# Optimization experiments

Hardware: AMD Instinct MI355X
Metric: run time of the kernel (lower is better)

## Reference

```python
import jax, jax.numpy as jnp
import numpy as np

E = 1024  # embed_dim
H = 16    # num_heads
D = E // H  # head_dim


def setup_inputs() -> dict:
    key = jax.random.key(0)
    ks = jax.random.split(key, 9)
    s = 0.02
    return {
        "hidden_state": jax.random.normal(ks[0], (4, 1024, E), jnp.float32),
        "Wq": jax.random.normal(ks[1], (H, D, E), jnp.float32) * s,
        "bq": jax.random.normal(ks[2], (H, D), jnp.float32) * s,
        "Wk": jax.random.normal(ks[3], (H, D, E), jnp.float32) * s,
        "bk": jax.random.normal(ks[4], (H, D), jnp.float32) * s,
        "Wv": jax.random.normal(ks[5], (H, D, E), jnp.float32) * s,
        "bv": jax.random.normal(ks[6], (H, D), jnp.float32) * s,
        "Wo": jax.random.normal(ks[7], (E, E), jnp.float32) * s,
        "bo": jax.random.normal(ks[8], (E,), jnp.float32) * s,
    }


def _mha(x, Wq, bq, Wk, bk, Wv, bv, Wo, bo):
    # Per-head linear projections (torch Linear: y = x W^T + b), batched over heads.
    q = jnp.einsum("bse,hde->bhsd", x, Wq) + bq[None, :, None, :]
    k = jnp.einsum("bse,hde->bhsd", x, Wk) + bk[None, :, None, :]
    v = jnp.einsum("bse,hde->bhsd", x, Wv) + bv[None, :, None, :]
    scores = jnp.einsum("bhsd,bhtd->bhst", q, k) / jnp.sqrt(jnp.asarray(D, x.dtype))
    w = jax.nn.softmax(scores, axis=-1)  # F.softmax default -> last dim
    o = jnp.einsum("bhst,bhtd->bhsd", w, v)
    # concat heads along last dim: [B,S,H*D] in head order (matches torch.cat)
    B, _, S, _ = o.shape
    o = jnp.transpose(o, (0, 2, 1, 3)).reshape(B, S, H * D)
    return o @ Wo.T + bo


def reference(hidden_state, Wq, bq, Wk, bk, Wv, bv, Wo, bo):
    return _mha(hidden_state, Wq, bq, Wk, bk, Wv, bv, Wo, bo)
```

## Files before the change

### kernel.cpp

```cpp
#include <hip/hip_runtime.h>
#include <hip/hip_bf16.h>
#include <stdint.h>

#define E_DIM 1024
#define H_NUM 16
#define D_DIM 64
#define B_NUM 4
#define S_LEN 1024

typedef __attribute__((ext_vector_type(8))) short bf16x8;
typedef __attribute__((ext_vector_type(4))) short bf16x4;
typedef __attribute__((ext_vector_type(4))) float f32x4;

#define SOFTMAX_C2 0.18033688011112042f

__device__ inline ushort f2b(float x) {
    __hip_bfloat16 h = __float2bfloat16(x);
    return *(ushort*)&h;
}
__device__ inline float b2f(ushort u) {
    __hip_bfloat16 h = *(__hip_bfloat16*)&u;
    return __bfloat162float(h);
}
__device__ inline uint pk2(float a, float b) {
    __hip_bfloat162 h = __float22bfloat162_rn(make_float2(a, b));
    return *(uint*)&h;
}

__device__ inline void gld16(const ushort* g, ushort* l) {
    __builtin_amdgcn_global_load_lds((const __attribute__((address_space(1))) void*)g,
                                     (__attribute__((address_space(3))) void*)l, 16, 0, 0);
}

__global__ __launch_bounds__(256)
void convert_all(const float* __restrict__ X,  const float* __restrict__ Wq,
                 const float* __restrict__ Wk, const float* __restrict__ Wv,
                 const float* __restrict__ Wo,
                 ushort* __restrict__ Xb, ushort* __restrict__ Wcat,
                 ushort* __restrict__ Wob)
{
    const int bid = blockIdx.x;
    const float* src; ushort* dst; size_t off;
    if (bid < 4096)      { src = X;  dst = Xb;   off = (size_t)bid * 1024; }
    else if (bid < 5120) { src = Wq; dst = Wcat;              off = (size_t)(bid - 4096) * 1024; }
    else if (bid < 6144) { src = Wk; dst = Wcat + (1u << 20); off = (size_t)(bid - 5120) * 1024; }
    else if (bid < 7168) { src = Wv; dst = Wcat + (2u << 20); off = (size_t)(bid - 6144) * 1024; }
    else                 { src = Wo; dst = Wob;               off = (size_t)(bid - 7168) * 1024; }
    const size_t i = off + (size_t)threadIdx.x * 4;
    float4 v = *(const float4*)&src[i];
    ushort4 o;
    o.x = f2b(v.x); o.y = f2b(v.y); o.z = f2b(v.z); o.w = f2b(v.w);
    *(ushort4*)&dst[i] = o;
}

__global__ __launch_bounds__(256, 3)
void gemm_qkv(const ushort* __restrict__ A, const ushort* __restrict__ Bw,
              const float* __restrict__ b0, const float* __restrict__ b1,
              const float* __restrict__ b2,
              ushort* __restrict__ Qb, ushort* __restrict__ Kb,
              ushort* __restrict__ Vt_g, int K)
{
    __shared__ __align__(16) ushort SM[24576];
    ushort* As = SM;
    ushort* Bs = SM + 16384;

    const int tid  = threadIdx.x;
    const int wave = tid >> 6;
    const int lane = tid & 63;
    const int quad = lane >> 4;
    const int l16  = lane & 15;
    const int wm   = wave & 1;
    const int wn   = wave >> 1;
    const int m0   = blockIdx.x * 128;
    const int n0   = blockIdx.y * 64;

    f32x4 acc[4][2] = {};

    auto stageA = [&](int buf, int k0) {
#pragma unroll
        for (int i = 0; i < 4; ++i) {
            const int e   = i * 256 + tid;
            const int row = e >> 3;
            const int gc8 = ((e & 7) ^ (row & 7)) * 8;
            gld16(&A[(size_t)(m0 + row) * K + k0 + gc8], &As[buf * 8192 + e * 8]);
        }
    };
    auto stageB = [&](int buf, int k0) {
#pragma unroll
        for (int i = 0; i < 2; ++i) {
            const int e   = i * 256 + tid;
            const int row = e >> 3;
            const int gc8 = ((e & 7) ^ (row & 7)) * 8;
            gld16(&Bw[(size_t)(n0 + row) * K + k0 + gc8], &Bs[buf * 4096 + e * 8]);
        }
    };

    stageA(0, 0); stageB(0, 0);
    __syncthreads();

    const int nk = K >> 6;
    const int xa = (l16 & 7) * 8;
    for (int ki = 0; ki < nk; ++ki) {
        const int cur = ki & 1;
        if (ki + 1 < nk) { stageA(cur ^ 1, (ki + 1) << 6); stageB(cur ^ 1, (ki + 1) << 6); }

#pragma unroll
        for (int ks = 0; ks < 2; ++ks) {
            const int lc = (ks * 32 + quad * 8) ^ xa;
            bf16x8 af[4], bf[2];
#pragma unroll
            for (int mi = 0; mi < 4; ++mi)
                af[mi] = *(const bf16x8*)&As[cur * 8192 + (wm * 64 + mi * 16 + l16) * 64 + lc];
#pragma unroll
            for (int ni = 0; ni < 2; ++ni)
                bf[ni] = *(const bf16x8*)&Bs[cur * 4096 + (wn * 32 + ni * 16 + l16) * 64 + lc];
#pragma unroll
            for (int mi = 0; mi < 4; ++mi)
#pragma unroll
                for (int ni = 0; ni < 2; ++ni)
                    acc[mi][ni] = __builtin_amdgcn_mfma_f32_16x16x32_bf16(af[mi], bf[ni], acc[mi][ni], 0, 0, 0);
        }
        __syncthreads();
    }

    const int seg   = n0 >> 10;
    const int cbase = n0 & 1023;
    const float* bp = (seg == 0) ? b0 : (seg == 1) ? b1 : b2;
    const float scl = (seg == 0) ? SOFTMAX_C2 : 1.0f;

    if (seg < 2) {
        ushort* T = SM;
#pragma unroll
        for (int ni = 0; ni < 2; ++ni) {
            const int nloc = wn * 32 + ni * 16 + l16;
            const float bv = bp[cbase + nloc];
#pragma unroll
            for (int mi = 0; mi < 4; ++mi)
#pragma unroll
                for (int r = 0; r < 4; ++r)
                    T[(wm * 64 + mi * 16 + quad * 4 + r) * 72 + nloc] =
                        f2b((acc[mi][ni][r] + bv) * scl);
        }
        __syncthreads();
        ushort* dst = (seg == 0) ? Qb : Kb;
        const int row = tid >> 1, half = tid & 1;
        const ushort* s = &T[row * 72 + half * 32];
        ushort* d = &dst[(size_t)(m0 + row) * 1024 + cbase + half * 32];
#pragma unroll
        for (int j = 0; j < 4; ++j)
            *(uint4*)(d + j * 8) = *(const uint4*)(s + j * 8);
    } else {
        ushort* Tt = SM;
        const int hh = cbase >> 6;
        const int b  = m0 >> 10, sbase = m0 & 1023;
#pragma unroll
        for (int ni = 0; ni < 2; ++ni) {
            const int nloc = wn * 32 + ni * 16 + l16;
            const float bv = bp[cbase + nloc];
#pragma unroll
            for (int mi = 0; mi < 4; ++mi) {
                const int mloc = wm * 64 + mi * 16 + quad * 4;
                ushort4 pk;
                pk.x = f2b(acc[mi][ni][0] + bv);
                pk.y = f2b(acc[mi][ni][1] + bv);
                pk.z = f2b(acc[mi][ni][2] + bv);
                pk.w = f2b(acc[mi][ni][3] + bv);
                *(ushort4*)&Tt[nloc * 136 + mloc] = pk;
            }
        }
        __syncthreads();
        const int nrow = tid >> 2, qtr = tid & 3;
        const ushort* s = &Tt[nrow * 136 + qtr * 32];
        ushort* d = &Vt_g[(((size_t)(b * 16 + hh)) * 64 + nrow) * 1024 + sbase + qtr * 32];
#pragma unroll
        for (int j = 0; j < 4; ++j)
            *(uint4*)(d + j * 8) = *(const uint4*)(s + j * 8);
    }
}

__global__ __launch_bounds__(256, 8)
void attention6(const ushort* __restrict__ Qg, const ushort* __restrict__ Kg,
                const ushort* __restrict__ Vg,
                ushort* __restrict__ Opart, float* __restrict__ Lpart)
{
    __shared__ ushort Kb[2][32][72];
    __shared__ ushort Vb[2][64][40];

    const int tid  = threadIdx.x;
    const int w    = tid >> 6;
    const int lane = tid & 63;
    const int quad = lane >> 4;
    const int l16  = lane & 15;

    const int qt = blockIdx.x;
    const int bh = blockIdx.y;
    const int th = blockIdx.z;
    const int b  = bh >> 4;
    const int h  = bh & 15;
    const size_t tbase = ((size_t)b * S_LEN) * E_DIM + (size_t)h * D_DIM;
    const size_t vbase = (size_t)bh * D_DIM * S_LEN;
    const int t0 = th * 512;

    const ushort* qrow = Qg + tbase + (size_t)(qt * 64 + w * 16 + l16) * E_DIM + quad * 8;
    bf16x8 qf[2];
    qf[0] = *(const bf16x8*)qrow;
    qf[1] = *(const bf16x8*)(qrow + 32);

    {
        const int kr = tid >> 3, kc = (tid & 7) * 8;
        *(uint4*)&Kb[0][kr][kc] = *(const uint4*)&Kg[tbase + (size_t)(t0 + kr) * E_DIM + kc];
        const int vr = tid >> 2, vc = (tid & 3) * 8;
        *(uint4*)&Vb[0][vr][vc] = *(const uint4*)&Vg[vbase + (size_t)vr * S_LEN + t0 + vc];
    }
    __syncthreads();

    float lq = 0.0f;
    f32x4 oacc[4] = {};

    for (int kt = 0; kt < 16; ++kt) {
        const int cur = kt & 1;

        uint4 kpre, vpre;
        const int kr = tid >> 3, kc = (tid & 7) * 8;
        const int vr = tid >> 2, vc = (tid & 3) * 8;
        if (kt < 15) {
            const int tg = t0 + (kt + 1) * 32;
            kpre = *(const uint4*)&Kg[tbase + (size_t)(tg + kr) * E_DIM + kc];
            vpre = *(const uint4*)&Vg[vbase + (size_t)vr * S_LEN + tg + vc];
        }

        f32x4 sacc[2] = {};
#pragma unroll
        for (int mt = 0; mt < 2; ++mt)
#pragma unroll
            for (int ks = 0; ks < 2; ++ks) {
                bf16x8 kf = *(const bf16x8*)&Kb[cur][mt * 16 + l16][ks * 32 + quad * 8];
                sacc[mt] = __builtin_amdgcn_mfma_f32_16x16x32_bf16(kf, qf[ks], sacc[mt], 0, 0, 0);
            }

        bf16x4 pf[2];
        float rs = 0.0f;
#pragma unroll
        for (int mt = 0; mt < 2; ++mt) {
            float p0 = exp2f(sacc[mt][0]);
            float p1 = exp2f(sacc[mt][1]);
            float p2 = exp2f(sacc[mt][2]);
            float p3 = exp2f(sacc[mt][3]);
            rs += (p0 + p1) + (p2 + p3);
            union { uint uu[2]; bf16x4 v; } pk;
            pk.uu[0] = pk2(p0, p1);
            pk.uu[1] = pk2(p2, p3);
            pf[mt] = pk.v;
        }
        lq += rs;

#pragma unroll
        for (int nb = 0; nb < 4; ++nb)
#pragma unroll
            for (int kb = 0; kb < 2; ++kb) {
                bf16x4 vf = *(const bf16x4*)&Vb[cur][nb * 16 + l16][kb * 16 + quad * 4];
                oacc[nb] = __builtin_amdgcn_mfma_f32_16x16x16bf16_1k(pf[kb], vf, oacc[nb], 0, 0, 0);
            }

        if (kt < 15) {
            const int nxt = cur ^ 1;
            *(uint4*)&Kb[nxt][kr][kc] = kpre;
            *(uint4*)&Vb[nxt][vr][vc] = vpre;
        }
        __syncthreads();
    }

    lq += __shfl_xor(lq, 16);
    lq += __shfl_xor(lq, 32);
    const size_t obase = ((size_t)(th * 64 + bh)) * S_LEN;
    if (lane < 16)
        Lpart[obase + qt * 64 + w * 16 + l16] = lq;

    ushort* T = &Kb[0][0][0];
#pragma unroll
    for (int nb = 0; nb < 4; ++nb)
#pragma unroll
        for (int r = 0; r < 4; ++r)
            T[(w * 16 + quad * 4 + r) * 72 + nb * 16 + l16] = f2b(oacc[nb][r]);
    __syncthreads();
    {
        const int row = tid >> 2, c16 = (tid & 3) * 16;
        const ushort* s = &T[row * 72 + c16];
        ushort* d = &Opart[(obase + qt * 64 + row) * 64 + c16];
        *(uint4*)(d)     = *(const uint4*)(s);
        *(uint4*)(d + 8) = *(const uint4*)(s + 8);
    }
}

__global__ __launch_bounds__(256, 3)
void gemm_out(const ushort* __restrict__ Opart, const float* __restrict__ Lpart,
              const ushort* __restrict__ Bw, const float* __restrict__ bias,
              float* __restrict__ Cout)
{
    __shared__ __align__(16) ushort SM[26624];
    ushort* As = SM;
    ushort* Bs = SM + 18432;

    const int tid  = threadIdx.x;
    const int wave = tid >> 6;
    const int lane = tid & 63;
    const int quad = lane >> 4;
    const int l16  = lane & 15;
    const int wm   = wave & 1;
    const int wn   = wave >> 1;
    const int m0   = blockIdx.x * 128;
    const int n0   = blockIdx.y * 64;

    const int arow = tid >> 1;
    const int ah   = (tid & 1) * 32;
    const int m    = m0 + arow;
    const int ab   = m >> 10;
    const int as   = m & 1023;

    f32x4 acc[4][2] = {};

    auto loadA = [&](int ki, uint4* o0, uint4* o1, float* linv) {
        const int bh = ab * 16 + ki;
        const size_t p0 = ((size_t)bh * 1024 + as) * 64 + ah;
        const size_t p1 = ((size_t)(64 + bh) * 1024 + as) * 64 + ah;
#pragma unroll
        for (int j = 0; j < 4; ++j) {
            o0[j] = *(const uint4*)&Opart[p0 + j * 8];
            o1[j] = *(const uint4*)&Opart[p1 + j * 8];
        }
        const float l0 = Lpart[(size_t)bh * 1024 + as];
        const float l1 = Lpart[(size_t)(64 + bh) * 1024 + as];
        *linv = 1.0f / (l0 + l1);
    };
    auto writeA = [&](int buf, const uint4* o0, const uint4* o1, float linv) {
        ushort* dst = &As[buf * 9216 + arow * 72 + ah];
#pragma unroll
        for (int j = 0; j < 4; ++j) {
            const ushort* a = (const ushort*)&o0[j];
            const ushort* c = (const ushort*)&o1[j];
            union { uint uu[4]; uint4 v; } pk;
            pk.uu[0] = pk2((b2f(a[0]) + b2f(c[0])) * linv, (b2f(a[1]) + b2f(c[1])) * linv);
            pk.uu[1] = pk2((b2f(a[2]) + b2f(c[2])) * linv, (b2f(a[3]) + b2f(c[3])) * linv);
            pk.uu[2] = pk2((b2f(a[4]) + b2f(c[4])) * linv, (b2f(a[5]) + b2f(c[5])) * linv);
            pk.uu[3] = pk2((b2f(a[6]) + b2f(c[6])) * linv, (b2f(a[7]) + b2f(c[7])) * linv);
            *(uint4*)(dst + j * 8) = pk.v;
        }
    };
    auto stageB = [&](int buf, int k0) {
#pragma unroll
        for (int i = 0; i < 2; ++i) {
            const int e   = i * 256 + tid;
            const int row = e >> 3;
            const int gc8 = ((e & 7) ^ (row & 7)) * 8;
            gld16(&Bw[(size_t)(n0 + row) * 1024 + k0 + gc8], &Bs[buf * 4096 + e * 8]);
        }
    };

    {
        uint4 o0[4], o1[4]; float linv;
        loadA(0, o0, o1, &linv);
        writeA(0, o0, o1, linv);
        stageB(0, 0);
    }
    __syncthreads();

    const int xa = (l16 & 7) * 8;
    for (int ki = 0; ki < 16; ++ki) {
        const int cur = ki & 1;

        uint4 o0[4], o1[4]; float linv;
        if (ki + 1 < 16) {
            loadA(ki + 1, o0, o1, &linv);
            stageB(cur ^ 1, (ki + 1) << 6);
        }

#pragma unroll
        for (int ks = 0; ks < 2; ++ks) {
            const int lcB = (ks * 32 + quad * 8) ^ xa;
            bf16x8 af[4], bf[2];
#pragma unroll
            for (int mi = 0; mi < 4; ++mi)
                af[mi] = *(const bf16x8*)&As[cur * 9216 + (wm * 64 + mi * 16 + l16) * 72 + ks * 32 + quad * 8];
#pragma unroll
            for (int ni = 0; ni < 2; ++ni)
                bf[ni] = *(const bf16x8*)&Bs[cur * 4096 + (wn * 32 + ni * 16 + l16) * 64 + lcB];
#pragma unroll
            for (int mi = 0; mi < 4; ++mi)
#pragma unroll
                for (int ni = 0; ni < 2; ++ni)
                    acc[mi][ni] = __builtin_amdgcn_mfma_f32_16x16x32_bf16(af[mi], bf[ni], acc[mi][ni], 0, 0, 0);
        }

        if (ki + 1 < 16) writeA(cur ^ 1, o0, o1, linv);
        __syncthreads();
    }

    float* Tf = (float*)SM;
    float bv[2];
#pragma unroll
    for (int ni = 0; ni < 2; ++ni)
        bv[ni] = bias[n0 + wn * 32 + ni * 16 + l16];
#pragma unroll
    for (int p = 0; p < 2; ++p) {
        if (wm == p) {
#pragma unroll
            for (int ni = 0; ni < 2; ++ni) {
                const int nloc = wn * 32 + ni * 16 + l16;
#pragma unroll
                for (int mi = 0; mi < 4; ++mi)
#pragma unroll
                    for (int r = 0; r < 4; ++r)
                        Tf[(mi * 16 + quad * 4 + r) * 68 + nloc] = acc[mi][ni][r] + bv[ni];
            }
        }
        __syncthreads();
        const int row = tid >> 2, c16 = (tid & 3) * 16;
        const float* s = &Tf[row * 68 + c16];
        float* d = &Cout[(size_t)(m0 + p * 64 + row) * 1024 + n0 + c16];
#pragma unroll
        for (int j = 0; j < 4; ++j)
            *(float4*)(d + j * 4) = *(const float4*)(s + j * 4);
        __syncthreads();
    }
}

extern "C" void kernel_launch(void* const* d_in, const int* in_sizes, int n_in,
                              void* d_out, int out_size, void* d_ws, size_t ws_size,
                              hipStream_t stream)
{
    (void)in_sizes; (void)n_in; (void)out_size; (void)ws_size;

    const float* X  = (const float*)d_in[0];
    const float* Wq = (const float*)d_in[1];
    const float* bq = (const float*)d_in[2];
    const float* Wk = (const float*)d_in[3];
    const float* bk = (const float*)d_in[4];
    const float* Wv = (const float*)d_in[5];
    const float* bv = (const float*)d_in[6];
    const float* Wo = (const float*)d_in[7];
    const float* bo = (const float*)d_in[8];

    const size_t MEG = 1u << 20;
    ushort* ws    = (ushort*)d_ws;
    ushort* Xb    = ws;
    ushort* Wcat  = ws + 4 * MEG;
    ushort* Wob   = ws + 7 * MEG;
    ushort* Qb    = ws + 8 * MEG;
    ushort* Kb    = ws + 12 * MEG;
    ushort* Vtg   = ws + 16 * MEG;
    ushort* Opart = ws + 20 * MEG;
    float*  Lpart = (float*)(ws + 28 * MEG);

    dim3 blk(256);

    convert_all<<<8192, blk, 0, stream>>>(X, Wq, Wk, Wv, Wo, Xb, Wcat, Wob);

    gemm_qkv<<<dim3(32, 48), blk, 0, stream>>>(Xb, Wcat, bq, bk, bv,
                                               Qb, Kb, Vtg, E_DIM);

    attention6<<<dim3(16, 64, 2), blk, 0, stream>>>(Qb, Kb, Vtg, Opart, Lpart);

    gemm_out<<<dim3(32, 16), blk, 0, stream>>>(Opart, Lpart, Wob, bo,
                                               (float*)d_out);
}
```

Measured before the change: 201.5 us.

## Stage K tiles via direct global-to-LDS loads with swizzle; remap grid; shrink output GEMM tile

The attention kernel now stages K tiles with a direct global-to-LDS load helper (gld16) into an XOR-swizzled LDS layout, so K no longer passes through registers. It also flattens the grid to 1D with a remapped block index that groups the query tiles of one (batch, head, half) together for cache locality. The output GEMM drops from 128x64 to 64x64 tiles with one 16-row slice per wave, doubling the block count and raising the occupancy hint. Smaller tiles reduce per-block reuse of the weight tile, and correctness depends on gld16 ordering against the barrier.

```diff
diff --git a/kernel.cpp b/kernel.cpp
--- a/kernel.cpp
+++ b/kernel.cpp
@@ -179,12 +179,11 @@
 }
 
 __global__ __launch_bounds__(256, 8)
-void attention6(const ushort* __restrict__ Qg, const ushort* __restrict__ Kg,
+void attention7(const ushort* __restrict__ Qg, const ushort* __restrict__ Kg,
                 const ushort* __restrict__ Vg,
                 ushort* __restrict__ Opart, float* __restrict__ Lpart)
 {
-    __shared__ ushort Kb[2][32][72];
-    __shared__ ushort Vb[2][64][40];
+    __shared__ __align__(16) ushort SM[9216];
 
     const int tid  = threadIdx.x;
     const int w    = tid >> 6;
@@ -192,11 +191,13 @@
     const int quad = lane >> 4;
     const int l16  = lane & 15;
 
-    const int qt = blockIdx.x;
-    const int bh = blockIdx.y;
-    const int th = blockIdx.z;
-    const int b  = bh >> 4;
-    const int h  = bh & 15;
+    const int gid = blockIdx.x;
+    const int qt  = (gid >> 3) & 15;
+    const int grp = (gid & 7) | ((gid >> 7) << 3);
+    const int bh  = grp & 63;
+    const int th  = grp >> 6;
+    const int b   = bh >> 4;
+    const int h   = bh & 15;
     const size_t tbase = ((size_t)b * S_LEN) * E_DIM + (size_t)h * D_DIM;
     const size_t vbase = (size_t)bh * D_DIM * S_LEN;
     const int t0 = th * 512;
@@ -206,26 +207,32 @@
     qf[0] = *(const bf16x8*)qrow;
     qf[1] = *(const bf16x8*)(qrow + 32);
 
+    const int krow = tid >> 3, kslot = tid & 7;
+    const int vr   = tid >> 2, vc = (tid & 3) * 8;
+
+    auto stageK = [&](int buf, int tg) {
+        gld16(&Kg[tbase + (size_t)(tg + krow) * E_DIM + ((kslot ^ (krow & 7)) * 8)],
+              &SM[buf * 2048 + tid * 8]);
+    };
+
+    stageK(0, t0);
     {
-        const int kr = tid >> 3, kc = (tid & 7) * 8;
-        *(uint4*)&Kb[0][kr][kc] = *(const uint4*)&Kg[tbase + (size_t)(t0 + kr) * E_DIM + kc];
-        const int vr = tid >> 2, vc = (tid & 3) * 8;
-        *(uint4*)&Vb[0][vr][vc] = *(const uint4*)&Vg[vbase + (size_t)vr * S_LEN + t0 + vc];
+        uint4 v0 = *(const uint4*)&Vg[vbase + (size_t)vr * S_LEN + t0 + vc];
+        *(uint4*)&SM[4096 + vr * 40 + vc] = v0;
     }
     __syncthreads();
 
     float lq = 0.0f;
     f32x4 oacc[4] = {};
+    const int xk = (l16 & 7);
 
     for (int kt = 0; kt < 16; ++kt) {
         const int cur = kt & 1;
 
-        uint4 kpre, vpre;
-        const int kr = tid >> 3, kc = (tid & 7) * 8;
-        const int vr = tid >> 2, vc = (tid & 3) * 8;
+        uint4 vpre;
         if (kt < 15) {
             const int tg = t0 + (kt + 1) * 32;
-            kpre = *(const uint4*)&Kg[tbase + (size_t)(tg + kr) * E_DIM + kc];
+            stageK(cur ^ 1, tg);
             vpre = *(const uint4*)&Vg[vbase + (size_t)vr * S_LEN + tg + vc];
         }
 
@@ -234,7 +241,8 @@
         for (int mt = 0; mt < 2; ++mt)
 #pragma unroll
             for (int ks = 0; ks < 2; ++ks) {
-                bf16x8 kf = *(const bf16x8*)&Kb[cur][mt * 16 + l16][ks * 32 + quad * 8];
+                bf16x8 kf = *(const bf16x8*)&SM[cur * 2048 + (mt * 16 + l16) * 64 +
+                                                (((ks * 4 + quad) ^ xk) * 8)];
                 sacc[mt] = __builtin_amdgcn_mfma_f32_16x16x32_bf16(kf, qf[ks], sacc[mt], 0, 0, 0);
             }
 
@@ -258,15 +266,13 @@
         for (int nb = 0; nb < 4; ++nb)
 #pragma unroll
             for (int kb = 0; kb < 2; ++kb) {
-                bf16x4 vf = *(const bf16x4*)&Vb[cur][nb * 16 + l16][kb * 16 + quad * 4];
+                bf16x4 vf = *(const bf16x4*)&SM[4096 + cur * 2560 +
+                                                (nb * 16 + l16) * 40 + kb * 16 + quad * 4];
                 oacc[nb] = __builtin_amdgcn_mfma_f32_16x16x16bf16_1k(pf[kb], vf, oacc[nb], 0, 0, 0);
             }
 
-        if (kt < 15) {
-            const int nxt = cur ^ 1;
-            *(uint4*)&Kb[nxt][kr][kc] = kpre;
-            *(uint4*)&Vb[nxt][vr][vc] = vpre;
-        }
+        if (kt < 15)
+            *(uint4*)&SM[4096 + (cur ^ 1) * 2560 + vr * 40 + vc] = vpre;
         __syncthreads();
     }
 
@@ -276,7 +282,7 @@
     if (lane < 16)
         Lpart[obase + qt * 64 + w * 16 + l16] = lq;
 
-    ushort* T = &Kb[0][0][0];
+    ushort* T = SM;
 #pragma unroll
     for (int nb = 0; nb < 4; ++nb)
 #pragma unroll
@@ -292,39 +298,37 @@
     }
 }
 
-__global__ __launch_bounds__(256, 3)
+__global__ __launch_bounds__(256, 4)
 void gemm_out(const ushort* __restrict__ Opart, const float* __restrict__ Lpart,
               const ushort* __restrict__ Bw, const float* __restrict__ bias,
               float* __restrict__ Cout)
 {
-    __shared__ __align__(16) ushort SM[26624];
+    __shared__ __align__(16) ushort SM[17408];
     ushort* As = SM;
-    ushort* Bs = SM + 18432;
+    ushort* Bs = SM + 9216;
 
     const int tid  = threadIdx.x;
-    const int wave = tid >> 6;
+    const int w    = tid >> 6;
     const int lane = tid & 63;
     const int quad = lane >> 4;
     const int l16  = lane & 15;
-    const int wm   = wave & 1;
-    const int wn   = wave >> 1;
-    const int m0   = blockIdx.x * 128;
+    const int m0   = blockIdx.x * 64;
     const int n0   = blockIdx.y * 64;
 
-    const int arow = tid >> 1;
-    const int ah   = (tid & 1) * 32;
+    const int arow = tid >> 2;
+    const int acol = (tid & 3) * 16;
     const int m    = m0 + arow;
     const int ab   = m >> 10;
     const int as   = m & 1023;
 
-    f32x4 acc[4][2] = {};
+    f32x4 acc[4] = {};
 
     auto loadA = [&](int ki, uint4* o0, uint4* o1, float* linv) {
         const int bh = ab * 16 + ki;
-        const size_t p0 = ((size_t)bh * 1024 + as) * 64 + ah;
-        const size_t p1 = ((size_t)(64 + bh) * 1024 + as) * 64 + ah;
-#pragma unroll
-        for (int j = 0; j < 4; ++j) {
+        const size_t p0 = ((size_t)bh * 1024 + as) * 64 + acol;
+        const size_t p1 = ((size_t)(64 + bh) * 1024 + as) * 64 + acol;
+#pragma unroll
+        for (int j = 0; j < 2; ++j) {
             o0[j] = *(const uint4*)&Opart[p0 + j * 8];
             o1[j] = *(const uint4*)&Opart[p1 + j * 8];
         }
@@ -333,9 +337,9 @@
         *linv = 1.0f / (l0 + l1);
     };
     auto writeA = [&](int buf, const uint4* o0, const uint4* o1, float linv) {
-        ushort* dst = &As[buf * 9216 + arow * 72 + ah];
-#pragma unroll
-        for (int j = 0; j < 4; ++j) {
+        ushort* dst = &As[buf * 4608 + arow * 72 + acol];
+#pragma unroll
+        for (int j = 0; j < 2; ++j) {
             const ushort* a = (const ushort*)&o0[j];
             const ushort* c = (const ushort*)&o1[j];
             union { uint uu[4]; uint4 v; } pk;
@@ -357,7 +361,7 @@
     };
 
     {
-        uint4 o0[4], o1[4]; float linv;
+        uint4 o0[2], o1[2]; float linv;
         loadA(0, o0, o1, &linv);
         writeA(0, o0, o1, linv);
         stageB(0, 0);
@@ -368,7 +372,7 @@
     for (int ki = 0; ki < 16; ++ki) {
         const int cur = ki & 1;
 
-        uint4 o0[4], o1[4]; float linv;
+        uint4 o0[2], o1[2]; float linv;
         if (ki + 1 < 16) {
             loadA(ki + 1, o0, o1, &linv);
             stageB(cur ^ 1, (ki + 1) << 6);
@@ -376,19 +380,13 @@
 
 #pragma unroll
         for (int ks = 0; ks < 2; ++ks) {
-            const int lcB = (ks * 32 + quad * 8) ^ xa;
-            bf16x8 af[4], bf[2];
-#pragma unroll
-            for (int mi = 0; mi < 4; ++mi)
-                af[mi] = *(const bf16x8*)&As[cur * 9216 + (wm * 64 + mi * 16 + l16) * 72 + ks * 32 + quad * 8];
-#pragma unroll
-            for (int ni = 0; ni < 2; ++ni)
-                bf[ni] = *(const bf16x8*)&Bs[cur * 4096 + (wn * 32 + ni * 16 + l16) * 64 + lcB];
-#pragma unroll
-            for (int mi = 0; mi < 4; ++mi)
-#pragma unroll
-                for (int ni = 0; ni < 2; ++ni)
-                    acc[mi][ni] = __builtin_amdgcn_mfma_f32_16x16x32_bf16(af[mi], bf[ni], acc[mi][ni], 0, 0, 0);
+            bf16x8 af = *(const bf16x8*)&As[cur * 4608 + (w * 16 + l16) * 72 + ks * 32 + quad * 8];
+#pragma unroll
+            for (int nb = 0; nb < 4; ++nb) {
+                const int lcB = (ks * 32 + quad * 8) ^ xa;
+                bf16x8 bf = *(const bf16x8*)&Bs[cur * 4096 + (nb * 16 + l16) * 64 + lcB];
+                acc[nb] = __builtin_amdgcn_mfma_f32_16x16x32_bf16(af, bf, acc[nb], 0, 0, 0);
+            }
         }
 
         if (ki + 1 < 16) writeA(cur ^ 1, o0, o1, linv);
@@ -396,31 +394,21 @@
     }
 
     float* Tf = (float*)SM;
-    float bv[2];
-#pragma unroll
-    for (int ni = 0; ni < 2; ++ni)
-        bv[ni] = bias[n0 + wn * 32 + ni * 16 + l16];
-#pragma unroll
-    for (int p = 0; p < 2; ++p) {
-        if (wm == p) {
-#pragma unroll
-            for (int ni = 0; ni < 2; ++ni) {
-                const int nloc = wn * 32 + ni * 16 + l16;
-#pragma unroll
-                for (int mi = 0; mi < 4; ++mi)
-#pragma unroll
-                    for (int r = 0; r < 4; ++r)
-                        Tf[(mi * 16 + quad * 4 + r) * 68 + nloc] = acc[mi][ni][r] + bv[ni];
-            }
-        }
-        __syncthreads();
+#pragma unroll
+    for (int nb = 0; nb < 4; ++nb) {
+        const float bv = bias[n0 + nb * 16 + l16];
+#pragma unroll
+        for (int r = 0; r < 4; ++r)
+            Tf[(w * 16 + quad * 4 + r) * 68 + nb * 16 + l16] = acc[nb][r] + bv;
+    }
+    __syncthreads();
+    {
         const int row = tid >> 2, c16 = (tid & 3) * 16;
         const float* s = &Tf[row * 68 + c16];
-        float* d = &Cout[(size_t)(m0 + p * 64 + row) * 1024 + n0 + c16];
+        float* d = &Cout[(size_t)(m0 + row) * 1024 + n0 + c16];
 #pragma unroll
         for (int j = 0; j < 4; ++j)
             *(float4*)(d + j * 4) = *(const float4*)(s + j * 4);
-        __syncthreads();
     }
 }
 
@@ -458,8 +446,8 @@
     gemm_qkv<<<dim3(32, 48), blk, 0, stream>>>(Xb, Wcat, bq, bk, bv,
                                                Qb, Kb, Vtg, E_DIM);
 
-    attention6<<<dim3(16, 64, 2), blk, 0, stream>>>(Qb, Kb, Vtg, Opart, Lpart);
-
-    gemm_out<<<dim3(32, 16), blk, 0, stream>>>(Opart, Lpart, Wob, bo,
+    attention7<<<2048, blk, 0, stream>>>(Qb, Kb, Vtg, Opart, Lpart);
+
+    gemm_out<<<dim3(64, 16), blk, 0, stream>>>(Opart, Lpart, Wob, bo,
                                                (float*)d_out);
 }
```

After: 187.4 us. 1.08x faster.
